# Kernel tuning notes

Measured on AMD Instinct MI355X. Metric: run time of the kernel, lower is better.

## Reference

```python
import jax, jax.numpy as jnp
import numpy as np

NUM_QUBITS = 13
NUM_LAYERS = 2


def setup_inputs() -> dict:
    key = jax.random.key(0)
    k1, k2 = jax.random.split(key)
    x = jax.random.normal(k1, (512, 2 ** NUM_QUBITS), dtype=jnp.float32)
    weights = jax.random.normal(k2, (NUM_LAYERS, NUM_QUBITS, 3), dtype=jnp.float32)
    return {"x": x, "weights": weights}


def _rot_matrix(phi, theta, omega):
    # qml.Rot(phi, theta, omega) = RZ(omega) @ RY(theta) @ RZ(phi)
    c = jnp.cos(theta * 0.5).astype(jnp.complex64)
    s = jnp.sin(theta * 0.5).astype(jnp.complex64)
    e_m = jnp.exp((-0.5j) * (phi + omega).astype(jnp.complex64))
    e_p = jnp.exp((0.5j) * (phi + omega).astype(jnp.complex64))
    e_d = jnp.exp((0.5j) * (phi - omega).astype(jnp.complex64))
    e_dc = jnp.exp((-0.5j) * (phi - omega).astype(jnp.complex64))
    row0 = jnp.stack([e_m * c, -e_d * s])
    row1 = jnp.stack([e_dc * s, e_p * c])
    return jnp.stack([row0, row1])  # (2, 2) complex64


def _apply_1q(psi, U, q):
    # psi: (B, 2, 2, ..., 2); contract qubit axis q with 2x2 gate U
    ax = 1 + q
    psi = jnp.moveaxis(psi, ax, -1)
    psi = psi @ U.T
    return jnp.moveaxis(psi, -1, ax)


def _apply_cnot(psi, c, t):
    # X on target where control bit == 1
    s0 = jax.lax.index_in_dim(psi, 0, axis=1 + c, keepdims=True)
    s1 = jax.lax.index_in_dim(psi, 1, axis=1 + c, keepdims=True)
    s1 = jnp.flip(s1, axis=1 + t)
    return jnp.concatenate([s0, s1], axis=1 + c)


def reference(x, weights):
    n = NUM_QUBITS
    B = x.shape[0]
    # AmplitudeEmbedding with normalize=True
    norm = jnp.sqrt(jnp.sum(x * x, axis=1, keepdims=True))
    psi = (x / norm).astype(jnp.complex64).reshape((B,) + (2,) * n)
    # StronglyEntanglingLayers (default ranges r_l = (l % (n-1)) + 1, CNOT imprimitive)
    for l in range(NUM_LAYERS):
        r = (l % (n - 1)) + 1
        for q in range(n):
            U = _rot_matrix(weights[l, q, 0], weights[l, q, 1], weights[l, q, 2])
            psi = _apply_1q(psi, U, q)
        for q in range(n):
            psi = _apply_cnot(psi, q, (q + r) % n)
    # expval(PauliZ(n // 2)) = p(bit=0) - p(bit=1)
    m = n // 2
    probs = jnp.real(psi) ** 2 + jnp.imag(psi) ** 2
    axes = tuple(i for i in range(1, n + 1) if i != 1 + m)
    p = probs.sum(axis=axes)  # (B, 2)
    return p[:, 0] - p[:, 1]
```

## Files before the change

### kernel.cpp

```cpp
#include <hip/hip_runtime.h>
#include <math.h>

#define NQ    13
#define DIM   8192
#define BLOCK 512
#define NGATE 26


__device__ __forceinline__ int SW(int a) { return a ^ (((a >> 7) & 7) << 2); }

struct PCols { int c[NQ]; };
constexpr PCols make_cols(int r) {
    PCols P{};
    for (int b = 0; b < NQ; ++b) {
        int cc = 1 << b;
        for (int cq = 0; cq < NQ; ++cq) {
            const int cb = 12 - cq;
            const int tb = 12 - ((cq + r) % NQ);
            cc ^= ((cc >> cb) & 1) << tb;
        }
        P.c[b] = cc;
    }
    return P;
}
constexpr PCols C1 = make_cols(1);
constexpr int make_rm6() {
    int m = 0;
    for (int b = 0; b < NQ; ++b) m |= ((make_cols(2).c[b] >> 6) & 1) << b;
    return m;
}
constexpr int RM6 = make_rm6();

struct Combos { int k[16]; };
constexpr Combos make_combos() {
    Combos K{};
    for (int j = 0; j < 16; ++j)
        K.k[j] = ((j & 1) ? C1.c[0] : 0) ^ ((j & 2) ? C1.c[1] : 0)
               ^ ((j & 4) ? C1.c[10] : 0) ^ ((j & 8) ? C1.c[11] : 0);
    return K;
}
constexpr Combos KC = make_combos();

constexpr int make_sjw() {
    int wv = 0;
    for (int j = 0; j < 16; ++j) {
        const int jm = (j & 3) | (((j >> 2) & 3) << 10);
        wv |= (__builtin_popcount(jm & RM6) & 1) << j;
    }
    return wv;
}
constexpr int SJW = make_sjw();

__device__ __forceinline__ float2 f2mul(float s, float2 a) {
    return make_float2(s * a.x, s * a.y);
}
__device__ __forceinline__ float2 f2fma(float s, float2 a, float2 b) {
    return make_float2(fmaf(s, a.x, b.x), fmaf(s, a.y, b.y));
}
__device__ __forceinline__ float2 fswap(float2 a) { return make_float2(-a.y, a.x); }

struct G8 { float4 a, b; };
__device__ __forceinline__ G8 ldg8(const float* gm, int gi) {
    G8 g;
    g.a = *(const float4*)&gm[gi * 8];
    g.b = *(const float4*)&gm[gi * 8 + 4];
    return g;
}

template<int P>
__device__ __forceinline__ void rotp(float2* c, const G8 g) {
    #pragma unroll
    for (int m = 0; m < 8; ++m) {
        const int j0 = ((m >> P) << (P + 1)) | (m & ((1 << P) - 1));
        const int j1 = j0 | (1 << P);
        const float2 a0 = c[j0], a1 = c[j1];
        const float2 s0 = fswap(a0), s1 = fswap(a1);
        c[j0] = f2fma(g.a.w, s1, f2fma(g.a.z, a1, f2fma(g.a.y, s0, f2mul(g.a.x, a0))));
        c[j1] = f2fma(g.b.w, s1, f2fma(g.b.z, a1, f2fma(g.b.y, s0, f2mul(g.b.x, a0))));
    }
}

template<int CTRL>
__device__ __forceinline__ float dppx(float v) {
    return __int_as_float(
        __builtin_amdgcn_update_dpp(0, __float_as_int(v), CTRL, 0xf, 0xf, true));
}
template<int CTRL>
__device__ __forceinline__ void rotlane(float2* c, const G8 g, const bool hi) {
    const float Ar = hi ? g.b.z : g.a.x;
    const float Ai = hi ? g.b.w : g.a.y;
    const float Br = hi ? g.b.x : g.a.z;
    const float Bi = hi ? g.b.y : g.a.w;
    #pragma unroll
    for (int j = 0; j < 16; ++j) {
        const float2 p  = make_float2(dppx<CTRL>(c[j].x), dppx<CTRL>(c[j].y));
        const float2 so = fswap(c[j]), sp = fswap(p);
        c[j] = f2fma(Bi, sp, f2fma(Br, p, f2fma(Ai, so, f2mul(Ar, c[j]))));
    }
}

__device__ __forceinline__ void loadgrp(const float* re, const float* im, int a, float2* c) {
    const float4 r = *(const float4*)&re[a];
    const float4 i = *(const float4*)&im[a];
    c[0] = make_float2(r.x, i.x); c[1] = make_float2(r.y, i.y);
    c[2] = make_float2(r.z, i.z); c[3] = make_float2(r.w, i.w);
}
__device__ __forceinline__ void storegrp(float* re, float* im, int a, const float2* c) {
    *(float4*)&re[a] = make_float4(c[0].x, c[1].x, c[2].x, c[3].x);
    *(float4*)&im[a] = make_float4(c[0].y, c[1].y, c[2].y, c[3].y);
}

__global__ __launch_bounds__(BLOCK, 4) void qsim_kernel(
    const float* __restrict__ x,
    const float* __restrict__ w,
    float* __restrict__ out)
{
    __shared__ __align__(16) float re[DIM];
    __shared__ __align__(16) float im[DIM];
    __shared__ __align__(16) float gm[NGATE * 8];
    __shared__ float red_ss[8], red_acc[8];

    const int b = blockIdx.x;
    const int t = threadIdx.x;

    if (t < NGATE) {
        const float phi = w[t * 3 + 0], theta = w[t * 3 + 1], omega = w[t * 3 + 2];
        float co, si;  sincosf(0.5f * theta, &si, &co);
        float sps, cps, sds, cds;
        sincosf(0.5f * (phi + omega), &sps, &cps);
        sincosf(0.5f * (phi - omega), &sds, &cds);
        float* g = &gm[t * 8];
        g[0] =  cps * co;  g[1] = -sps * co;
        g[2] = -cds * si;  g[3] = -sds * si;
        g[4] =  cds * si;  g[5] = -sds * si;
        g[6] =  cps * co;  g[7] =  sps * co;
    }

    const float4* x4 = (const float4*)(x + (size_t)b * DIM);
    float2 c[16];
    float ss = 0.f;
    #pragma unroll
    for (int g = 0; g < 4; ++g) {
        const float4 v = x4[(t << 2) | g];
        c[4 * g + 0] = make_float2(v.x, 0.f);
        c[4 * g + 1] = make_float2(v.y, 0.f);
        c[4 * g + 2] = make_float2(v.z, 0.f);
        c[4 * g + 3] = make_float2(v.w, 0.f);
        ss += v.x * v.x + v.y * v.y + v.z * v.z + v.w * v.w;
    }
    #pragma unroll
    for (int off = 32; off > 0; off >>= 1) ss += __shfl_down(ss, off, 64);
    if ((t & 63) == 0) red_ss[t >> 6] = ss;
    __syncthreads();
    float total = 0.f;
    #pragma unroll
    for (int i = 0; i < 8; ++i) total += red_ss[i];

    const int base2 = (((t >> 2) & 15) << 2) | ((t & 3) << 8) | (((t >> 6) & 7) << 10);
    const int base3 = (((t >> 1) & 255) << 2) | ((t & 1) << 12);

    #pragma unroll
    for (int l = 0; l < 2; ++l) {
        const int G = l * 13;

        if (l != 0) {
            #pragma unroll
            for (int g = 0; g < 4; ++g)
                loadgrp(re, im, SW((t << 4) | (g << 2)), &c[4 * g]);
        }
        rotp<0>(c, ldg8(gm, G + 12));
        rotp<1>(c, ldg8(gm, G + 11));
        rotp<2>(c, ldg8(gm, G + 10));
        rotp<3>(c, ldg8(gm, G +  9));
        rotlane<0xB1>(c, ldg8(gm, G + 8), (t & 1) != 0);
        rotlane<0x4E>(c, ldg8(gm, G + 7), (t & 2) != 0);
        #pragma unroll
        for (int g = 0; g < 4; ++g)
            storegrp(re, im, SW((t << 4) | (g << 2)), &c[4 * g]);
        __syncthreads();

        #pragma unroll
        for (int h = 0; h < 4; ++h) loadgrp(re, im, SW(base2 | (h << 6)), &c[4 * h]);
        rotp<2>(c, ldg8(gm, G + 6));
        rotp<3>(c, ldg8(gm, G + 5));
        rotlane<0xB1>(c, ldg8(gm, G + 4), (t & 1) != 0);
        rotlane<0x4E>(c, ldg8(gm, G + 3), (t & 2) != 0);
        #pragma unroll
        for (int h = 0; h < 4; ++h) storegrp(re, im, SW(base2 | (h << 6)), &c[4 * h]);
        __syncthreads();

        #pragma unroll
        for (int h = 0; h < 4; ++h) loadgrp(re, im, SW(base3 | (h << 10)), &c[4 * h]);
        if (l == 0) __syncthreads();
        rotp<2>(c, ldg8(gm, G + 2));
        rotp<3>(c, ldg8(gm, G + 1));
        rotlane<0xB1>(c, ldg8(gm, G + 0), (t & 1) != 0);

        if (l == 0) {
            int mb = 0;
            if (t & 1) mb ^= C1.c[12];
            #pragma unroll
            for (int bb = 0; bb < 8; ++bb)
                if ((t >> (bb + 1)) & 1) mb ^= C1.c[2 + bb];
            #pragma unroll
            for (int j = 0; j < 16; ++j) {
                const int a = SW(mb ^ KC.k[j]);
                re[a] = c[j].x; im[a] = c[j].y;
            }
            __syncthreads();
        }
    }

    const int sbase = __popc(base3 & RM6) & 1;
    float acc = 0.f;
    #pragma unroll
    for (int j = 0; j < 16; ++j) {
        const float p = c[j].x * c[j].x + c[j].y * c[j].y;
        acc += (sbase ^ ((SJW >> j) & 1)) ? -p : p;
    }
    #pragma unroll
    for (int off = 32; off > 0; off >>= 1) acc += __shfl_down(acc, off, 64);
    if ((t & 63) == 0) red_acc[t >> 6] = acc;
    __syncthreads();
    if (t == 0) {
        float tot = 0.f;
        #pragma unroll
        for (int i = 0; i < 8; ++i) tot += red_acc[i];
        out[b] = tot / total;
    }
}

extern "C" void kernel_launch(void* const* d_in, const int* in_sizes, int n_in,
                              void* d_out, int out_size, void* d_ws, size_t ws_size,
                              hipStream_t stream) {
    const float* x = (const float*)d_in[0];
    const float* w = (const float*)d_in[1];
    float* out = (float*)d_out;
    const int B = in_sizes[0] / DIM;
    qsim_kernel<<<B, BLOCK, 0, stream>>>(x, w, out);
}
```

Baseline: 85.92 us.

## Double threads per block, halve amplitudes per thread with DPP cross-lane gates

Moves from 512 threads holding 16 amplitudes each to 1024 threads holding 8 each. More qubits are now handled across lanes with DPP permutes, including two-step mirror/reverse combinations for lane bits 2 and 3. The index mappings for the second and third LDS passes and the CNOT scatter are redone to match. The aim is more parallelism and latency hiding per block, at the cost of extra DPP ops and a larger reduction across 16 waves. The 64KB LDS per block still allows only a couple of blocks per CU.

```diff
diff --git a/kernel.cpp b/kernel.cpp
--- a/kernel.cpp
+++ b/kernel.cpp
@@ -3,7 +3,7 @@
 
 #define NQ    13
 #define DIM   8192
-#define BLOCK 512
+#define BLOCK 1024
 #define NGATE 26
 
 
@@ -31,20 +31,20 @@
 }
 constexpr int RM6 = make_rm6();
 
-struct Combos { int k[16]; };
+struct Combos { int k[8]; };
 constexpr Combos make_combos() {
     Combos K{};
-    for (int j = 0; j < 16; ++j)
+    for (int j = 0; j < 8; ++j)
         K.k[j] = ((j & 1) ? C1.c[0] : 0) ^ ((j & 2) ? C1.c[1] : 0)
-               ^ ((j & 4) ? C1.c[10] : 0) ^ ((j & 8) ? C1.c[11] : 0);
+               ^ ((j & 4) ? C1.c[10] : 0);
     return K;
 }
 constexpr Combos KC = make_combos();
 
 constexpr int make_sjw() {
     int wv = 0;
-    for (int j = 0; j < 16; ++j) {
-        const int jm = (j & 3) | (((j >> 2) & 3) << 10);
+    for (int j = 0; j < 8; ++j) {
+        const int jm = (j & 3) | (((j >> 2) & 1) << 10);
         wv |= (__builtin_popcount(jm & RM6) & 1) << j;
     }
     return wv;
@@ -70,7 +70,7 @@
 template<int P>
 __device__ __forceinline__ void rotp(float2* c, const G8 g) {
     #pragma unroll
-    for (int m = 0; m < 8; ++m) {
+    for (int m = 0; m < 4; ++m) {
         const int j0 = ((m >> P) << (P + 1)) | (m & ((1 << P) - 1));
         const int j1 = j0 | (1 << P);
         const float2 a0 = c[j0], a1 = c[j1];
@@ -80,20 +80,32 @@
     }
 }
 
+#define DPP_XOR1 0xB1
+#define DPP_XOR2 0x4E
+#define DPP_QREV 0x1B
+#define DPP_HMIR 0x141
+#define DPP_MIR  0x140
+
 template<int CTRL>
-__device__ __forceinline__ float dppx(float v) {
+__device__ __forceinline__ float dpp1(float v) {
     return __int_as_float(
         __builtin_amdgcn_update_dpp(0, __float_as_int(v), CTRL, 0xf, 0xf, true));
 }
-template<int CTRL>
+template<int CA, int CB>
+__device__ __forceinline__ float dppx(float v) {
+    float r = dpp1<CA>(v);
+    if constexpr (CB >= 0) r = dpp1<CB>(r);
+    return r;
+}
+template<int CA, int CB>
 __device__ __forceinline__ void rotlane(float2* c, const G8 g, const bool hi) {
     const float Ar = hi ? g.b.z : g.a.x;
     const float Ai = hi ? g.b.w : g.a.y;
     const float Br = hi ? g.b.x : g.a.z;
     const float Bi = hi ? g.b.y : g.a.w;
     #pragma unroll
-    for (int j = 0; j < 16; ++j) {
-        const float2 p  = make_float2(dppx<CTRL>(c[j].x), dppx<CTRL>(c[j].y));
+    for (int j = 0; j < 8; ++j) {
+        const float2 p  = make_float2(dppx<CA, CB>(c[j].x), dppx<CA, CB>(c[j].y));
         const float2 so = fswap(c[j]), sp = fswap(p);
         c[j] = f2fma(Bi, sp, f2fma(Br, p, f2fma(Ai, so, f2mul(Ar, c[j]))));
     }
@@ -110,7 +122,7 @@
     *(float4*)&im[a] = make_float4(c[0].y, c[1].y, c[2].y, c[3].y);
 }
 
-__global__ __launch_bounds__(BLOCK, 4) void qsim_kernel(
+__global__ __launch_bounds__(BLOCK, 8) void qsim_kernel(
     const float* __restrict__ x,
     const float* __restrict__ w,
     float* __restrict__ out)
@@ -118,7 +130,7 @@
     __shared__ __align__(16) float re[DIM];
     __shared__ __align__(16) float im[DIM];
     __shared__ __align__(16) float gm[NGATE * 8];
-    __shared__ float red_ss[8], red_acc[8];
+    __shared__ float red_ss[16], red_acc[16];
 
     const int b = blockIdx.x;
     const int t = threadIdx.x;
@@ -137,11 +149,11 @@
     }
 
     const float4* x4 = (const float4*)(x + (size_t)b * DIM);
-    float2 c[16];
+    float2 c[8];
     float ss = 0.f;
     #pragma unroll
-    for (int g = 0; g < 4; ++g) {
-        const float4 v = x4[(t << 2) | g];
+    for (int g = 0; g < 2; ++g) {
+        const float4 v = x4[(t << 1) | g];
         c[4 * g + 0] = make_float2(v.x, 0.f);
         c[4 * g + 1] = make_float2(v.y, 0.f);
         c[4 * g + 2] = make_float2(v.z, 0.f);
@@ -152,12 +164,13 @@
     for (int off = 32; off > 0; off >>= 1) ss += __shfl_down(ss, off, 64);
     if ((t & 63) == 0) red_ss[t >> 6] = ss;
     __syncthreads();
-    float total = 0.f;
-    #pragma unroll
-    for (int i = 0; i < 8; ++i) total += red_ss[i];
-
-    const int base2 = (((t >> 2) & 15) << 2) | ((t & 3) << 8) | (((t >> 6) & 7) << 10);
-    const int base3 = (((t >> 1) & 255) << 2) | ((t & 1) << 12);
+
+    const int base2 = (((t >> 4) & 1) << 2) | (((t >> 5) & 1) << 3)
+                    | (((t >> 6) & 1) << 4) | ((t & 1) << 6)
+                    | (((t >> 1) & 1) << 7) | (((t >> 2) & 1) << 8)
+                    | (((t >> 3) & 1) << 9) | (((t >> 7) & 1) << 10)
+                    | (((t >> 8) & 1) << 11) | (((t >> 9) & 1) << 12);
+    const int base3 = (((t >> 2) & 255) << 2) | ((t & 1) << 11) | (((t >> 1) & 1) << 12);
 
     #pragma unroll
     for (int l = 0; l < 2; ++l) {
@@ -165,45 +178,49 @@
 
         if (l != 0) {
             #pragma unroll
-            for (int g = 0; g < 4; ++g)
-                loadgrp(re, im, SW((t << 4) | (g << 2)), &c[4 * g]);
+            for (int g = 0; g < 2; ++g)
+                loadgrp(re, im, SW((t << 3) | (g << 2)), &c[4 * g]);
         }
         rotp<0>(c, ldg8(gm, G + 12));
         rotp<1>(c, ldg8(gm, G + 11));
         rotp<2>(c, ldg8(gm, G + 10));
-        rotp<3>(c, ldg8(gm, G +  9));
-        rotlane<0xB1>(c, ldg8(gm, G + 8), (t & 1) != 0);
-        rotlane<0x4E>(c, ldg8(gm, G + 7), (t & 2) != 0);
-        #pragma unroll
-        for (int g = 0; g < 4; ++g)
-            storegrp(re, im, SW((t << 4) | (g << 2)), &c[4 * g]);
+        rotlane<DPP_XOR1, -1>(c, ldg8(gm, G + 9), (t & 1) != 0);
+        rotlane<DPP_XOR2, -1>(c, ldg8(gm, G + 8), (t & 2) != 0);
+        #pragma unroll
+        for (int g = 0; g < 2; ++g)
+            storegrp(re, im, SW((t << 3) | (g << 2)), &c[4 * g]);
         __syncthreads();
 
         #pragma unroll
-        for (int h = 0; h < 4; ++h) loadgrp(re, im, SW(base2 | (h << 6)), &c[4 * h]);
-        rotp<2>(c, ldg8(gm, G + 6));
-        rotp<3>(c, ldg8(gm, G + 5));
-        rotlane<0xB1>(c, ldg8(gm, G + 4), (t & 1) != 0);
-        rotlane<0x4E>(c, ldg8(gm, G + 3), (t & 2) != 0);
-        #pragma unroll
-        for (int h = 0; h < 4; ++h) storegrp(re, im, SW(base2 | (h << 6)), &c[4 * h]);
+        for (int g = 0; g < 2; ++g)
+            loadgrp(re, im, SW(base2 | (g << 5)), &c[4 * g]);
+        rotp<2>(c, ldg8(gm, G + 7));
+        rotlane<DPP_XOR1, -1>(c, ldg8(gm, G + 6), (t & 1) != 0);
+        rotlane<DPP_XOR2, -1>(c, ldg8(gm, G + 5), (t & 2) != 0);
+        rotlane<DPP_HMIR, DPP_QREV>(c, ldg8(gm, G + 4), (t & 4) != 0);
+        rotlane<DPP_MIR,  DPP_HMIR>(c, ldg8(gm, G + 3), (t & 8) != 0);
+        #pragma unroll
+        for (int g = 0; g < 2; ++g)
+            storegrp(re, im, SW(base2 | (g << 5)), &c[4 * g]);
         __syncthreads();
 
         #pragma unroll
-        for (int h = 0; h < 4; ++h) loadgrp(re, im, SW(base3 | (h << 10)), &c[4 * h]);
+        for (int g = 0; g < 2; ++g)
+            loadgrp(re, im, SW(base3 | (g << 10)), &c[4 * g]);
         if (l == 0) __syncthreads();
         rotp<2>(c, ldg8(gm, G + 2));
-        rotp<3>(c, ldg8(gm, G + 1));
-        rotlane<0xB1>(c, ldg8(gm, G + 0), (t & 1) != 0);
+        rotlane<DPP_XOR1, -1>(c, ldg8(gm, G + 1), (t & 1) != 0);
+        rotlane<DPP_XOR2, -1>(c, ldg8(gm, G + 0), (t & 2) != 0);
 
         if (l == 0) {
             int mb = 0;
-            if (t & 1) mb ^= C1.c[12];
+            if (t & 1) mb ^= C1.c[11];
+            if (t & 2) mb ^= C1.c[12];
             #pragma unroll
             for (int bb = 0; bb < 8; ++bb)
-                if ((t >> (bb + 1)) & 1) mb ^= C1.c[2 + bb];
+                if ((t >> (bb + 2)) & 1) mb ^= C1.c[2 + bb];
             #pragma unroll
-            for (int j = 0; j < 16; ++j) {
+            for (int j = 0; j < 8; ++j) {
                 const int a = SW(mb ^ KC.k[j]);
                 re[a] = c[j].x; im[a] = c[j].y;
             }
@@ -214,7 +231,7 @@
     const int sbase = __popc(base3 & RM6) & 1;
     float acc = 0.f;
     #pragma unroll
-    for (int j = 0; j < 16; ++j) {
+    for (int j = 0; j < 8; ++j) {
         const float p = c[j].x * c[j].x + c[j].y * c[j].y;
         acc += (sbase ^ ((SJW >> j) & 1)) ? -p : p;
     }
@@ -223,10 +240,10 @@
     if ((t & 63) == 0) red_acc[t >> 6] = acc;
     __syncthreads();
     if (t == 0) {
-        float tot = 0.f;
-        #pragma unroll
-        for (int i = 0; i < 8; ++i) tot += red_acc[i];
-        out[b] = tot / total;
+        float ta = 0.f, ts = 0.f;
+        #pragma unroll
+        for (int i = 0; i < 16; ++i) { ta += red_acc[i]; ts += red_ss[i]; }
+        out[b] = ta / ts;
     }
 }
 
```

Result: slower. 88.79 us (+3.3%).
